# Performance work log

Hardware: AMD Instinct MI355X
Metric: run time of the kernel (lower is better)

## Reference

```python
import jax, jax.numpy as jnp
import numpy as np

T = 8192
N_EMBD = 1024
HEAD_SIZE = 64
NEG_FILL = -1e9


def setup_inputs() -> dict:
    key = jax.random.key(0)
    kq, kk, kv, kwq, kwk, kwv = jax.random.split(key, 6)
    s = 1.0 / np.sqrt(N_EMBD)
    return {
        "encodings_for_q": jax.random.normal(kq, (T, N_EMBD), dtype=jnp.float32),
        "encodings_for_k": jax.random.normal(kk, (T, N_EMBD), dtype=jnp.float32),
        "encodings_for_v": jax.random.normal(kv, (T, N_EMBD), dtype=jnp.float32),
        # causal mask: True above the diagonal -> positions to mask out
        "mask": jnp.triu(jnp.ones((T, T), dtype=bool), k=1),
        # torch Linear weights have shape [out_features, in_features]
        "W_q": jax.random.normal(kwq, (HEAD_SIZE, N_EMBD), dtype=jnp.float32) * s,
        "W_k": jax.random.normal(kwk, (HEAD_SIZE, N_EMBD), dtype=jnp.float32) * s,
        "W_v": jax.random.normal(kwv, (HEAD_SIZE, N_EMBD), dtype=jnp.float32) * s,
    }


def reference(encodings_for_q, encodings_for_k, encodings_for_v, mask, W_q, W_k, W_v):
    # projections: x @ W.T  (torch nn.Linear, bias=False)
    q = jnp.einsum("te,he->th", encodings_for_q, W_q)  # [T, H]
    k = jnp.einsum("te,he->th", encodings_for_k, W_k)  # [T, H]
    v = jnp.einsum("te,he->th", encodings_for_v, W_v)  # [T, H]
    scale = 1.0 / jnp.sqrt(jnp.asarray(HEAD_SIZE, dtype=q.dtype))
    sims = jnp.einsum("th,sh->ts", q, k) * scale       # [T, T]
    sims = jnp.where(mask, jnp.asarray(NEG_FILL, dtype=sims.dtype), sims)
    attn = jax.nn.softmax(sims, axis=1)                # softmax over col_dim=1
    return jnp.einsum("ts,sh->th", attn, v)            # [T, H]
```

## Files before the change

### kernel.cpp

```cpp
#include <hip/hip_runtime.h>
#include <hip/hip_bf16.h>
#include <stdint.h>

#define T_DIM 8192
#define E_DIM 1024
#define H_DIM 64
#define NEGF  -3.0e38f
#define QSCALE 0.18033688011112042f

typedef __attribute__((ext_vector_type(8))) short bf16x8;
typedef __attribute__((ext_vector_type(4))) float f32x4;

static __device__ __forceinline__ uint32_t pk2(float x, float y) {
    __hip_bfloat162 h = __float22bfloat162_rn(make_float2(x, y));
    union { __hip_bfloat162 h2; uint32_t u; } c; c.h2 = h; return c.u;
}
static __device__ __forceinline__ bf16x8 pack8(float4 a, float4 b) {
    union { bf16x8 v; uint32_t u[4]; } c;
    c.u[0] = pk2(a.x, a.y); c.u[1] = pk2(a.z, a.w);
    c.u[2] = pk2(b.x, b.y); c.u[3] = pk2(b.z, b.w);
    return c.v;
}
static __device__ __forceinline__ uint16_t bf1(float x) {
    __hip_bfloat16 h = __float2bfloat16(x);
    union { __hip_bfloat16 h1; uint16_t s; } c; c.h1 = h; return c.s;
}

__global__ __launch_bounds__(256) void wconv_kernel(
    const float* __restrict__ Wq, const float* __restrict__ Wk, const float* __restrict__ Wv,
    uint16_t* __restrict__ Wqb, uint16_t* __restrict__ Wkb, uint16_t* __restrict__ Wvb)
{
    const int idx = blockIdx.x * 256 + threadIdx.x;
    const int which = idx / 16384;
    const int off = (idx & 16383) * 4;
    const float* W = (which == 0) ? Wq : (which == 1) ? Wk : Wv;
    uint16_t* Wb   = (which == 0) ? Wqb : (which == 1) ? Wkb : Wvb;
    const float s  = (which == 0) ? QSCALE : 1.0f;
    float4 w = *(const float4*)(W + off);
    uint2 o = make_uint2(pk2(w.x * s, w.y * s), pk2(w.z * s, w.w * s));
    *(uint2*)(Wb + off) = o;
}

__global__ __launch_bounds__(256) void proj_kernel(
    const float* __restrict__ Xq, const float* __restrict__ Xk, const float* __restrict__ Xv,
    const uint16_t* __restrict__ Wqb, const uint16_t* __restrict__ Wkb, const uint16_t* __restrict__ Wvb,
    uint16_t* __restrict__ Qb, uint16_t* __restrict__ Kb, uint16_t* __restrict__ Vtb)
{
    __shared__ float PS[2][16][68];
    __shared__ float TD[32][69];

    const int mat = blockIdx.y;
    const float* X    = (mat == 0) ? Xq  : (mat == 1) ? Xk  : Xv;
    const uint16_t* W = (mat == 0) ? Wqb : (mat == 1) ? Wkb : Wvb;

    const int tid  = threadIdx.x;
    const int wv   = tid >> 6;
    const int rs   = wv & 1;
    const int kh   = wv >> 1;
    const int lane = tid & 63;
    const int lidx = lane & 15;
    const int quad = lane >> 4;
    const int t0   = blockIdx.x * 32 + rs * 16;

    const float*    Xr  = X + (size_t)(t0 + lidx) * E_DIM + kh * 512 + quad * 8;
    const uint16_t* Wr0 = W + (size_t)lidx * E_DIM + kh * 512 + quad * 8;

    f32x4 acc[4] = {{0,0,0,0},{0,0,0,0},{0,0,0,0},{0,0,0,0}};
    #pragma unroll 2
    for (int k0 = 0; k0 < 512; k0 += 64) {
        float4 x0 = *(const float4*)(Xr + k0);
        float4 x1 = *(const float4*)(Xr + k0 + 4);
        float4 x2 = *(const float4*)(Xr + k0 + 32);
        float4 x3 = *(const float4*)(Xr + k0 + 36);
        bf16x8 xa0 = pack8(x0, x1);
        bf16x8 xa1 = pack8(x2, x3);
        #pragma unroll
        for (int nt = 0; nt < 4; ++nt) {
            const uint16_t* wr = Wr0 + (size_t)nt * 16 * E_DIM + k0;
            bf16x8 wb0 = *(const bf16x8*)wr;
            bf16x8 wb1 = *(const bf16x8*)(wr + 32);
            acc[nt] = __builtin_amdgcn_mfma_f32_16x16x32_bf16(xa0, wb0, acc[nt], 0, 0, 0);
            acc[nt] = __builtin_amdgcn_mfma_f32_16x16x32_bf16(xa1, wb1, acc[nt], 0, 0, 0);
        }
    }

    if (kh) {
        #pragma unroll
        for (int nt = 0; nt < 4; ++nt)
            #pragma unroll
            for (int r = 0; r < 4; ++r)
                PS[rs][quad * 4 + r][nt * 16 + lidx] = acc[nt][r];
    }
    __syncthreads();
    if (!kh) {
        #pragma unroll
        for (int nt = 0; nt < 4; ++nt)
            #pragma unroll
            for (int r = 0; r < 4; ++r)
                acc[nt][r] += PS[rs][quad * 4 + r][nt * 16 + lidx];

        if (mat < 2) {
            uint16_t* O = (mat == 0) ? Qb : Kb;
            #pragma unroll
            for (int nt = 0; nt < 4; ++nt)
                #pragma unroll
                for (int r = 0; r < 4; ++r)
                    O[(size_t)(t0 + quad * 4 + r) * H_DIM + nt * 16 + lidx] = bf1(acc[nt][r]);
        } else {
            #pragma unroll
            for (int nt = 0; nt < 4; ++nt)
                #pragma unroll
                for (int r = 0; r < 4; ++r)
                    TD[rs * 16 + quad * 4 + r][nt * 16 + lidx] = acc[nt][r];
        }
    }
    if (mat == 2) {
        __syncthreads();
        const int h = tid >> 2, tq = tid & 3;
        uint32_t w8[4];
        #pragma unroll
        for (int i = 0; i < 4; ++i)
            w8[i] = pk2(TD[tq * 8 + 2 * i][h], TD[tq * 8 + 2 * i + 1][h]);
        uint16_t* dst = Vtb + (size_t)h * T_DIM + blockIdx.x * 32 + tq * 8;
        *(uint4*)dst = make_uint4(w8[0], w8[1], w8[2], w8[3]);
    }
}

__global__ __launch_bounds__(512, 4) void flash_kernel(
    const uint16_t* __restrict__ Qb, const uint16_t* __restrict__ Kb,
    const uint16_t* __restrict__ Vtb, float* __restrict__ Out)
{
    __shared__ __align__(16) float WS[8][16][68];
    __shared__ float Lw[8][16];

    const int tid  = threadIdx.x;
    const int wv   = tid >> 6;
    const int lane = tid & 63;
    const int lidx = lane & 15;
    const int quad = lane >> 4;

    const int qt = 511 - (int)blockIdx.x;
    const int q0 = qt * 16;

    bf16x8 aq0 = *(const bf16x8*)(Qb + (size_t)(q0 + lidx) * H_DIM + quad * 8);
    bf16x8 aq1 = *(const bf16x8*)(Qb + (size_t)(q0 + lidx) * H_DIM + 32 + quad * 8);

    const int ktiles  = qt / 4 + 1;
    const int base    = ktiles >> 3;
    const int rem     = ktiles & 7;
    const int myn     = base + (wv < rem ? 1 : 0);
    const int mystart = wv * base + (wv < rem ? wv : rem);

    float l[4] = {0.f, 0.f, 0.f, 0.f};
    f32x4 o[4] = {{0,0,0,0},{0,0,0,0},{0,0,0,0},{0,0,0,0}};

    const uint16_t* Kl = Kb  + (size_t)lidx * H_DIM + quad * 8;
    const uint16_t* Vl = Vtb + (size_t)lidx * T_DIM + quad * 8;

    for (int it = 0; it < myn; ++it) {
        const int kt = mystart + it;
        const int s0 = kt * 64;

        bf16x8 vb[8];
        #pragma unroll
        for (int nt = 0; nt < 4; ++nt) {
            const uint16_t* vr = Vl + (size_t)(nt * 16) * T_DIM + s0;
            vb[2 * nt]     = *(const bf16x8*)vr;
            vb[2 * nt + 1] = *(const bf16x8*)(vr + 32);
        }

        bf16x8 kb[8];
        #pragma unroll
        for (int nt = 0; nt < 4; ++nt) {
            const uint16_t* kr = Kl + (size_t)(s0 + nt * 16) * H_DIM;
            kb[2 * nt]     = *(const bf16x8*)kr;
            kb[2 * nt + 1] = *(const bf16x8*)(kr + 32);
        }

        f32x4 s[4];
        __builtin_amdgcn_s_setprio(1);
        #pragma unroll
        for (int nt = 0; nt < 4; ++nt) {
            f32x4 z = {0, 0, 0, 0};
            s[nt] = __builtin_amdgcn_mfma_f32_16x16x32_bf16(aq0, kb[2 * nt],     z,     0, 0, 0);
            s[nt] = __builtin_amdgcn_mfma_f32_16x16x32_bf16(aq1, kb[2 * nt + 1], s[nt], 0, 0, 0);
        }
        __builtin_amdgcn_s_setprio(0);

        const bool dg = (kt == ktiles - 1);
        #pragma unroll
        for (int nt = 0; nt < 4; ++nt) {
            #pragma unroll
            for (int r = 0; r < 4; ++r) {
                float pv = exp2f(s[nt][r]);
                if (dg) {
                    const int col = s0 + nt * 16 + lidx;
                    const int row = q0 + quad * 4 + r;
                    pv = (col <= row) ? pv : 0.f;
                }
                s[nt][r] = pv;
                WS[wv][quad * 4 + r][nt * 16 + lidx] = pv;
            }
        }
        #pragma unroll
        for (int r = 0; r < 4; ++r)
            l[r] += (s[0][r] + s[1][r]) + (s[2][r] + s[3][r]);

        const float* pr = &WS[wv][lidx][0];
        float4 p0 = *(const float4*)(pr + quad * 8);
        float4 p1 = *(const float4*)(pr + quad * 8 + 4);
        float4 p2 = *(const float4*)(pr + 32 + quad * 8);
        float4 p3 = *(const float4*)(pr + 32 + quad * 8 + 4);
        bf16x8 ap0 = pack8(p0, p1);
        bf16x8 ap1 = pack8(p2, p3);

        __builtin_amdgcn_s_setprio(1);
        #pragma unroll
        for (int nt = 0; nt < 4; ++nt) {
            o[nt] = __builtin_amdgcn_mfma_f32_16x16x32_bf16(ap0, vb[2 * nt],     o[nt], 0, 0, 0);
            o[nt] = __builtin_amdgcn_mfma_f32_16x16x32_bf16(ap1, vb[2 * nt + 1], o[nt], 0, 0, 0);
        }
        __builtin_amdgcn_s_setprio(0);
    }

    #pragma unroll
    for (int r = 0; r < 4; ++r) {
        float ps = l[r];
        ps += __shfl_xor(ps, 1);
        ps += __shfl_xor(ps, 2);
        ps += __shfl_xor(ps, 4);
        ps += __shfl_xor(ps, 8);
        l[r] = ps;
    }

    if (lidx == 0) {
        #pragma unroll
        for (int r = 0; r < 4; ++r) Lw[wv][quad * 4 + r] = l[r];
    }
    #pragma unroll
    for (int nt = 0; nt < 4; ++nt)
        #pragma unroll
        for (int r = 0; r < 4; ++r)
            WS[wv][quad * 4 + r][nt * 16 + lidx] = o[nt][r];
    __syncthreads();

    const int row = tid >> 5, cg = tid & 31;
    float L = 0.f;
    float ox = 0.f, oy = 0.f;
    #pragma unroll
    for (int w2 = 0; w2 < 8; ++w2) {
        L += Lw[w2][row];
        float2 t = *(const float2*)&WS[w2][row][cg * 2];
        ox += t.x; oy += t.y;
    }
    const float inv = 1.f / L;
    *(float2*)(Out + (size_t)(q0 + row) * H_DIM + cg * 2) = make_float2(ox * inv, oy * inv);
}

extern "C" void kernel_launch(void* const* d_in, const int* in_sizes, int n_in,
                              void* d_out, int out_size, void* d_ws, size_t ws_size,
                              hipStream_t stream) {
    (void)in_sizes; (void)n_in; (void)out_size; (void)ws_size;
    const float* Xq = (const float*)d_in[0];
    const float* Xk = (const float*)d_in[1];
    const float* Xv = (const float*)d_in[2];
    const float* Wq = (const float*)d_in[4];
    const float* Wk = (const float*)d_in[5];
    const float* Wv = (const float*)d_in[6];

    uint16_t* Qb  = (uint16_t*)d_ws;
    uint16_t* Kb  = Qb + (size_t)T_DIM * H_DIM;
    uint16_t* Vtb = Kb + (size_t)T_DIM * H_DIM;
    uint16_t* Wqb = Vtb + (size_t)T_DIM * H_DIM;
    uint16_t* Wkb = Wqb + (size_t)H_DIM * E_DIM;
    uint16_t* Wvb = Wkb + (size_t)H_DIM * E_DIM;

    wconv_kernel<<<192, 256, 0, stream>>>(Wq, Wk, Wv, Wqb, Wkb, Wvb);

    dim3 pgrid(T_DIM / 32, 3);
    proj_kernel<<<pgrid, 256, 0, stream>>>(Xq, Xk, Xv, Wqb, Wkb, Wvb, Qb, Kb, Vtb);

    flash_kernel<<<T_DIM / 16, 512, 0, stream>>>(Qb, Kb, Vtb, (float*)d_out);
}
```

Measured before the change: 457.9 us.

## Fuse weight conversion into projection kernel and enlarge projection tiles

Drops the separate weight-conversion kernel launch. The projection kernel now reads fp32 weights directly, converts them to bf16 in registers, and applies the query scale on the X side. Blocks grow to 512 threads covering 64 rows, which halves the grid and gives each block more weight reuse. In exchange, every block reloads and reconverts fp32 weights, doubling weight traffic per MFMA, and the K loop now uses one MFMA per step instead of two.

Result: slower. 493.9 us (+7.9%).

```diff
diff --git a/kernel.cpp b/kernel.cpp
--- a/kernel.cpp
+++ b/kernel.cpp
@@ -21,66 +21,55 @@
     c.u[2] = pk2(b.x, b.y); c.u[3] = pk2(b.z, b.w);
     return c.v;
 }
+static __device__ __forceinline__ bf16x8 pack8s(float4 a, float4 b, float s) {
+    union { bf16x8 v; uint32_t u[4]; } c;
+    c.u[0] = pk2(a.x * s, a.y * s); c.u[1] = pk2(a.z * s, a.w * s);
+    c.u[2] = pk2(b.x * s, b.y * s); c.u[3] = pk2(b.z * s, b.w * s);
+    return c.v;
+}
 static __device__ __forceinline__ uint16_t bf1(float x) {
     __hip_bfloat16 h = __float2bfloat16(x);
     union { __hip_bfloat16 h1; uint16_t s; } c; c.h1 = h; return c.s;
 }
 
-__global__ __launch_bounds__(256) void wconv_kernel(
+__global__ __launch_bounds__(512) void proj_kernel(
+    const float* __restrict__ Xq, const float* __restrict__ Xk, const float* __restrict__ Xv,
     const float* __restrict__ Wq, const float* __restrict__ Wk, const float* __restrict__ Wv,
-    uint16_t* __restrict__ Wqb, uint16_t* __restrict__ Wkb, uint16_t* __restrict__ Wvb)
-{
-    const int idx = blockIdx.x * 256 + threadIdx.x;
-    const int which = idx / 16384;
-    const int off = (idx & 16383) * 4;
-    const float* W = (which == 0) ? Wq : (which == 1) ? Wk : Wv;
-    uint16_t* Wb   = (which == 0) ? Wqb : (which == 1) ? Wkb : Wvb;
-    const float s  = (which == 0) ? QSCALE : 1.0f;
-    float4 w = *(const float4*)(W + off);
-    uint2 o = make_uint2(pk2(w.x * s, w.y * s), pk2(w.z * s, w.w * s));
-    *(uint2*)(Wb + off) = o;
-}
-
-__global__ __launch_bounds__(256) void proj_kernel(
-    const float* __restrict__ Xq, const float* __restrict__ Xk, const float* __restrict__ Xv,
-    const uint16_t* __restrict__ Wqb, const uint16_t* __restrict__ Wkb, const uint16_t* __restrict__ Wvb,
     uint16_t* __restrict__ Qb, uint16_t* __restrict__ Kb, uint16_t* __restrict__ Vtb)
 {
-    __shared__ float PS[2][16][68];
-    __shared__ float TD[32][69];
+    __shared__ float PS[4][16][68];
+    __shared__ float TD[64][69];
 
     const int mat = blockIdx.y;
-    const float* X    = (mat == 0) ? Xq  : (mat == 1) ? Xk  : Xv;
-    const uint16_t* W = (mat == 0) ? Wqb : (mat == 1) ? Wkb : Wvb;
+    const float* X = (mat == 0) ? Xq : (mat == 1) ? Xk : Xv;
+    const float* W = (mat == 0) ? Wq : (mat == 1) ? Wk : Wv;
+    const float xs = (mat == 0) ? QSCALE : 1.0f;
 
     const int tid  = threadIdx.x;
     const int wv   = tid >> 6;
-    const int rs   = wv & 1;
-    const int kh   = wv >> 1;
+    const int rs   = wv & 3;
+    const int kh   = wv >> 2;
     const int lane = tid & 63;
     const int lidx = lane & 15;
     const int quad = lane >> 4;
-    const int t0   = blockIdx.x * 32 + rs * 16;
-
-    const float*    Xr  = X + (size_t)(t0 + lidx) * E_DIM + kh * 512 + quad * 8;
-    const uint16_t* Wr0 = W + (size_t)lidx * E_DIM + kh * 512 + quad * 8;
+    const int t0   = blockIdx.x * 64 + rs * 16;
+
+    const float* Xr  = X + (size_t)(t0 + lidx) * E_DIM + kh * 512 + quad * 8;
+    const float* Wr0 = W + (size_t)lidx * E_DIM + kh * 512 + quad * 8;
 
     f32x4 acc[4] = {{0,0,0,0},{0,0,0,0},{0,0,0,0},{0,0,0,0}};
-    #pragma unroll 2
-    for (int k0 = 0; k0 < 512; k0 += 64) {
+    #pragma unroll 4
+    for (int k0 = 0; k0 < 512; k0 += 32) {
         float4 x0 = *(const float4*)(Xr + k0);
         float4 x1 = *(const float4*)(Xr + k0 + 4);
-        float4 x2 = *(const float4*)(Xr + k0 + 32);
-        float4 x3 = *(const float4*)(Xr + k0 + 36);
-        bf16x8 xa0 = pack8(x0, x1);
-        bf16x8 xa1 = pack8(x2, x3);
-        #pragma unroll
-        for (int nt = 0; nt < 4; ++nt) {
-            const uint16_t* wr = Wr0 + (size_t)nt * 16 * E_DIM + k0;
-            bf16x8 wb0 = *(const bf16x8*)wr;
-            bf16x8 wb1 = *(const bf16x8*)(wr + 32);
-            acc[nt] = __builtin_amdgcn_mfma_f32_16x16x32_bf16(xa0, wb0, acc[nt], 0, 0, 0);
-            acc[nt] = __builtin_amdgcn_mfma_f32_16x16x32_bf16(xa1, wb1, acc[nt], 0, 0, 0);
+        bf16x8 xa = pack8s(x0, x1, xs);
+        #pragma unroll
+        for (int nt = 0; nt < 4; ++nt) {
+            const float* wr = Wr0 + (size_t)nt * 16 * E_DIM + k0;
+            float4 w0 = *(const float4*)wr;
+            float4 w1 = *(const float4*)(wr + 4);
+            bf16x8 wb = pack8(w0, w1);
+            acc[nt] = __builtin_amdgcn_mfma_f32_16x16x32_bf16(xa, wb, acc[nt], 0, 0, 0);
         }
     }
 
@@ -116,13 +105,18 @@
     }
     if (mat == 2) {
         __syncthreads();
-        const int h = tid >> 2, tq = tid & 3;
-        uint32_t w8[4];
-        #pragma unroll
-        for (int i = 0; i < 4; ++i)
-            w8[i] = pk2(TD[tq * 8 + 2 * i][h], TD[tq * 8 + 2 * i + 1][h]);
-        uint16_t* dst = Vtb + (size_t)h * T_DIM + blockIdx.x * 32 + tq * 8;
-        *(uint4*)dst = make_uint4(w8[0], w8[1], w8[2], w8[3]);
+        if (tid < 256) {
+            const int h = tid >> 2, tq = tid & 3;
+            uint32_t w8[8];
+            #pragma unroll
+            for (int i = 0; i < 8; ++i)
+                w8[i] = pk2(TD[tq * 16 + 2 * i][h], TD[tq * 16 + 2 * i + 1][h]);
+            uint16_t* dst = Vtb + (size_t)h * T_DIM + blockIdx.x * 64 + tq * 16;
+            uint4 lo = make_uint4(w8[0], w8[1], w8[2], w8[3]);
+            uint4 hi = make_uint4(w8[4], w8[5], w8[6], w8[7]);
+            *(uint4*)dst       = lo;
+            *(uint4*)(dst + 8) = hi;
+        }
     }
 }
 
@@ -271,14 +265,9 @@
     uint16_t* Qb  = (uint16_t*)d_ws;
     uint16_t* Kb  = Qb + (size_t)T_DIM * H_DIM;
     uint16_t* Vtb = Kb + (size_t)T_DIM * H_DIM;
-    uint16_t* Wqb = Vtb + (size_t)T_DIM * H_DIM;
-    uint16_t* Wkb = Wqb + (size_t)H_DIM * E_DIM;
-    uint16_t* Wvb = Wkb + (size_t)H_DIM * E_DIM;
-
-    wconv_kernel<<<192, 256, 0, stream>>>(Wq, Wk, Wv, Wqb, Wkb, Wvb);
-
-    dim3 pgrid(T_DIM / 32, 3);
-    proj_kernel<<<pgrid, 256, 0, stream>>>(Xq, Xk, Xv, Wqb, Wkb, Wvb, Qb, Kb, Vtb);
+
+    dim3 pgrid(T_DIM / 64, 3);
+    proj_kernel<<<pgrid, 512, 0, stream>>>(Xq, Xk, Xv, Wq, Wk, Wv, Qb, Kb, Vtb);
 
     flash_kernel<<<T_DIM / 16, 512, 0, stream>>>(Qb, Kb, Vtb, (float*)d_out);
 }
```
